# Performance work log

Measured on AMD Instinct MI355X. Metric: run time of the kernel, lower is better.

The kernel has to match this reference:

```python
import jax, jax.numpy as jnp
import numpy as np

N_NODES = 10000
N_EDGES = 160000
HID = 256
NBOND = 6
NATOM = 62
NLAYERS = 6


def _lin_init(key, fan_in, fan_out):
    # torch nn.Linear default: U(-1/sqrt(fan_in), 1/sqrt(fan_in))
    kw, kb = jax.random.split(key)
    bound = 1.0 / np.sqrt(fan_in)
    w = jax.random.uniform(kw, (fan_in, fan_out), jnp.float32, -bound, bound)
    b = jax.random.uniform(kb, (fan_out,), jnp.float32, -bound, bound)
    return w, b


def setup_inputs() -> dict:
    key = jax.random.key(0)
    ks = jax.random.split(key, 32)
    atom_features = jax.random.normal(ks[0], (N_NODES, NATOM), jnp.float32)
    edge_index = jax.random.randint(ks[1], (2, N_EDGES), 0, N_NODES, jnp.int64 if jax.config.jax_enable_x64 else jnp.int32)
    edge_features = jax.random.normal(ks[2], (N_EDGES, NBOND), jnp.float32)

    embed_w, embed_b = _lin_init(ks[3], NATOM, HID)

    msg_in = 2 * HID + NBOND  # 518
    mw1, mb1, mw2, mb2 = [], [], [], []
    uw1, ub1, uw2, ub2 = [], [], [], []
    for i in range(NLAYERS):
        k = jax.random.split(ks[4 + i], 4)
        w, b = _lin_init(k[0], msg_in, HID); mw1.append(w); mb1.append(b)
        w, b = _lin_init(k[1], HID, HID); mw2.append(w); mb2.append(b)
        w, b = _lin_init(k[2], 2 * HID, HID); uw1.append(w); ub1.append(b)
        w, b = _lin_init(k[3], HID, HID); uw2.append(w); ub2.append(b)

    r_w1, r_b1 = _lin_init(ks[20], HID, HID)
    r_w2, r_b2 = _lin_init(ks[21], HID, HID // 2)
    r_w3, r_b3 = _lin_init(ks[22], HID // 2, 1)

    return {
        "atom_features": atom_features,
        "edge_index": edge_index,
        "edge_features": edge_features,
        "embed_w": embed_w, "embed_b": embed_b,
        "msg_w1": jnp.stack(mw1), "msg_b1": jnp.stack(mb1),
        "msg_w2": jnp.stack(mw2), "msg_b2": jnp.stack(mb2),
        "upd_w1": jnp.stack(uw1), "upd_b1": jnp.stack(ub1),
        "upd_w2": jnp.stack(uw2), "upd_b2": jnp.stack(ub2),
        "r_w1": r_w1, "r_b1": r_b1,
        "r_w2": r_w2, "r_b2": r_b2,
        "r_w3": r_w3, "r_b3": r_b3,
    }


def _mlp2(x, w1, b1, w2, b2):
    return jnp.maximum(x @ w1 + b1, 0.0) @ w2 + b2


def reference(atom_features, edge_index, edge_features,
              embed_w, embed_b,
              msg_w1, msg_b1, msg_w2, msg_b2,
              upd_w1, upd_b1, upd_w2, upd_b2,
              r_w1, r_b1, r_w2, r_b2, r_w3, r_b3):
    src, dst = edge_index[0], edge_index[1]
    n = atom_features.shape[0]
    x = atom_features @ embed_w + embed_b  # [N, H]
    for l in range(msg_w1.shape[0]):
        # per-edge gather + concat -> message MLP
        msg_in = jnp.concatenate([x[src], x[dst], edge_features], axis=-1)  # [E, 2H+B]
        msgs = _mlp2(msg_in, msg_w1[l], msg_b1[l], msg_w2[l], msg_b2[l])  # [E, H]
        # scatter-add into dst nodes
        agg = jax.ops.segment_sum(msgs, dst, num_segments=n)  # [N, H]
        x = _mlp2(jnp.concatenate([x, agg], axis=-1), upd_w1[l], upd_b1[l], upd_w2[l], upd_b2[l])
    # readout (dropout is identity in eval mode)
    h = jnp.maximum(x @ r_w1 + r_b1, 0.0)
    h = jnp.maximum(h @ r_w2 + r_b2, 0.0)
    out = h @ r_w3 + r_b3  # [N, 1]
    return out.mean(axis=0)  # [1]
```

## Files before the change

kernel.cpp:

```cpp
#include <hip/hip_runtime.h>
#include <hip/hip_bf16.h>
#include <hip/hip_fp16.h>


#define HID 256

typedef _Float16 h8 __attribute__((ext_vector_type(8)));
typedef float f32x4 __attribute__((ext_vector_type(4)));

__device__ __forceinline__ void unpack_h8(const int4& r, float* f) {
    const __half2* h = reinterpret_cast<const __half2*>(&r);
#pragma unroll
    for (int k = 0; k < 4; ++k) {
        float2 t = __half22float2(h[k]);
        f[2 * k] = t.x;
        f[2 * k + 1] = t.y;
    }
}

__device__ __forceinline__ void unpack_h4(const int2& r, float* f) {
    const __half2* h = reinterpret_cast<const __half2*>(&r);
    float2 t0 = __half22float2(h[0]);
    float2 t1 = __half22float2(h[1]);
    f[0] = t0.x; f[1] = t0.y; f[2] = t1.x; f[3] = t1.y;
}

__device__ __forceinline__ void gld16(const void* g, void* l) {
    __builtin_amdgcn_global_load_lds(
        (const __attribute__((address_space(1))) void*)g,
        (__attribute__((address_space(3))) void*)l, 16, 0, 0);
}

__device__ __forceinline__ int swz(int row) { return (row + (row >> 2)) & 3; }


__global__ void hist_act_kernel(const int* __restrict__ dst, int* __restrict__ deg,
                                int E, const float* __restrict__ atom,
                                __half* __restrict__ atomH, int NA) {
    int i = blockIdx.x * blockDim.x + threadIdx.x;
    if (i < E) atomicAdd(&deg[dst[i]], 1);
    if (i < NA) {
        int r = i >> 3, seg = i & 7;
        h8 v;
#pragma unroll
        for (int j = 0; j < 8; ++j) {
            int c = seg * 8 + j;
            v[j] = (_Float16)((c < 62) ? atom[(size_t)r * 62 + c] : 0.f);
        }
        *reinterpret_cast<h8*>(&atomH[(size_t)r * 64 + seg * 8]) = v;
    }
}

__global__ __launch_bounds__(256) void scan_kernel(
    const int* __restrict__ deg, int* __restrict__ offs, float* __restrict__ degf, int n) {
    __shared__ int ws[4];
    const int t = threadIdx.x;
    const int lane = t & 63;
    const int w = t >> 6;
    const int per = (n + 255) / 256;
    const int s = t * per;
    const int e = min(s + per, n);
    int sum = 0;
    for (int i = s; i < e; ++i) sum += deg[i];
    int v = sum;
#pragma unroll
    for (int off = 1; off < 64; off <<= 1) {
        int u = __shfl_up(v, off, 64);
        if (lane >= off) v += u;
    }
    if (lane == 63) ws[w] = v;
    __syncthreads();
    if (t == 0) {
        int c = 0;
#pragma unroll
        for (int i = 0; i < 4; ++i) { int x = ws[i]; ws[i] = c; c += x; }
    }
    __syncthreads();
    int run = ws[w] + v - sum;
    for (int i = s; i < e; ++i) {
        int d = deg[i];
        offs[i] = run;
        degf[i] = (float)d;
        run += d;
    }
    if (e == n) offs[n] = run;
}


struct CDesc {
    const float* src;
    __half* dst;
    int Kreal, Kpad, srcN, tile0, dstStride;
};
struct CTab {
    CDesc d[32];
    int nd;
};

__device__ void convert_body(const CTab& tab, int bid) {
    int idx = 0;
    for (int i = 1; i < tab.nd; ++i)
        if (tab.d[i].tile0 <= bid) idx = i;
    const CDesc d = tab.d[idx];
    const int q = bid - d.tile0;
    const int ntN = d.srcN >> 6;
    const int kb = (q / ntN) * 32;
    const int nb = (q % ntN) * 64;
    const int n = nb + (threadIdx.x & 63);
    const int k0 = kb + (threadIdx.x >> 6) * 8;
    h8 v;
#pragma unroll
    for (int j = 0; j < 8; ++j) {
        int k = k0 + j;
        v[j] = (_Float16)((k < d.Kreal) ? d.src[(size_t)k * d.srcN + n] : 0.f);
    }
    *reinterpret_cast<h8*>(&d.dst[(size_t)n * d.dstStride + k0]) = v;
}

__global__ __launch_bounds__(256) void scatter_conv_kernel(
    const int* __restrict__ src, const int* __restrict__ dst,
    const int* __restrict__ offs, int* __restrict__ cursor,
    int* __restrict__ csr_src, const float* __restrict__ ef,
    __half* __restrict__ ef8, int E, int sblocks, CTab tab) {
    if ((int)blockIdx.x < sblocks) {
        int i = blockIdx.x * blockDim.x + threadIdx.x;
        if (i < E) {
            int d = dst[i];
            int pos = atomicAdd(&cursor[d], 1);
            int idx = offs[d] + pos;
            csr_src[idx] = src[i];
            const float* s6 = ef + (size_t)i * 6;
            unsigned short h[8];
#pragma unroll
            for (int j = 0; j < 6; ++j) h[j] = __half_as_ushort(__float2half_rn(s6[j]));
            h[6] = 0; h[7] = 0;
            int4 pk;
            pk.x = (int)(h[0] | ((unsigned)h[1] << 16));
            pk.y = (int)(h[2] | ((unsigned)h[3] << 16));
            pk.z = (int)(h[4] | ((unsigned)h[5] << 16));
            pk.w = (int)(h[6] | ((unsigned)h[7] << 16));
            *reinterpret_cast<int4*>(ef8 + (size_t)idx * 8) = pk;
        }
    } else {
        convert_body(tab, blockIdx.x - sblocks);
    }
}


struct BDesc { float* out; const float* base; const float* v1; const float* B1;
               const float* v2; const float* B2; };
struct BTab { BDesc d[31]; };


#define ASTR 40

struct FDesc { const float* U2; const __half* Wfb; __half* dst; int stride; };
struct FTab { FDesc d[22]; };

__device__ void fold_tile(unsigned char* ldsraw, const FDesc& dd, int t4) {
    _Float16* Ah = (_Float16*)ldsraw;
    _Float16* Bh = (_Float16*)(ldsraw + 64 * ASTR * 2);
    const int rowBase = (t4 >> 2) * 64;
    const int colBase = (t4 & 3) * 64;

    const int tid = threadIdx.x;
    const int lane = tid & 63;
    const int wave = tid >> 6;
    const int waveM = (wave >> 1) * 32;
    const int waveN = (wave & 1) * 32;
    const int m0 = lane & 15;
    const int quad = lane >> 4;
    const int sr = tid >> 2;
    const int sseg = tid & 3;

    const f32x4 z = {0.f, 0.f, 0.f, 0.f};
    f32x4 acc[2][2] = {{z, z}, {z, z}};

    for (int kb = 0; kb < 256; kb += 32) {
        {
            size_t off = (size_t)(rowBase + sr) * 256 + kb + sseg * 8;
            *reinterpret_cast<int4*>(&Ah[sr * ASTR + sseg * 8]) =
                *reinterpret_cast<const int4*>(&dd.Wfb[off]);
        }
        {
            const float* Bp = dd.U2 + (size_t)(colBase + sr) * 256 + kb + sseg * 8;
            float4 u0 = *reinterpret_cast<const float4*>(Bp);
            float4 u1 = *reinterpret_cast<const float4*>(Bp + 4);
            h8 v;
            v[0] = (_Float16)u0.x; v[1] = (_Float16)u0.y;
            v[2] = (_Float16)u0.z; v[3] = (_Float16)u0.w;
            v[4] = (_Float16)u1.x; v[5] = (_Float16)u1.y;
            v[6] = (_Float16)u1.z; v[7] = (_Float16)u1.w;
            *reinterpret_cast<h8*>(&Bh[sr * ASTR + sseg * 8]) = v;
        }
        __syncthreads();

        const h8 a0 = *reinterpret_cast<const h8*>(&Ah[(waveM + m0) * ASTR + quad * 8]);
        const h8 a1 = *reinterpret_cast<const h8*>(&Ah[(waveM + 16 + m0) * ASTR + quad * 8]);
        const h8 b0 = *reinterpret_cast<const h8*>(&Bh[(waveN + m0) * ASTR + quad * 8]);
        const h8 b1 = *reinterpret_cast<const h8*>(&Bh[(waveN + 16 + m0) * ASTR + quad * 8]);

        acc[0][0] = __builtin_amdgcn_mfma_f32_16x16x32_f16(a0, b0, acc[0][0], 0, 0, 0);
        acc[0][1] = __builtin_amdgcn_mfma_f32_16x16x32_f16(a0, b1, acc[0][1], 0, 0, 0);
        acc[1][0] = __builtin_amdgcn_mfma_f32_16x16x32_f16(a1, b0, acc[1][0], 0, 0, 0);
        acc[1][1] = __builtin_amdgcn_mfma_f32_16x16x32_f16(a1, b1, acc[1][1], 0, 0, 0);

        __syncthreads();
    }

#pragma unroll
    for (int tm = 0; tm < 2; ++tm)
#pragma unroll
        for (int reg = 0; reg < 4; ++reg) {
            int n = rowBase + waveM + tm * 16 + quad * 4 + reg;
#pragma unroll
            for (int tn = 0; tn < 2; ++tn) {
                int k = colBase + waveN + tn * 16 + m0;
                dd.dst[(size_t)n * dd.stride + k] = __float2half_rn(acc[tm][tn][reg]);
            }
        }
}


template <int TN>
__device__ void gemm_tile(
    unsigned char* lds, int bx, int by,
    const __half* __restrict__ A, int lda, const __half* __restrict__ A2,
    const __half* __restrict__ W, int K,
    const float* __restrict__ bias, const float* __restrict__ bias2,
    const float* __restrict__ rowscale,
    __half* __restrict__ C, int M, int Nc, int do_relu) {
    constexpr int BUF = 4096 + TN * 2048;

    const int tid = threadIdx.x;
    const int lane = tid & 63;
    const int wave = tid >> 6;
    const int m0 = lane & 15;
    const int quad = lane >> 4;
    const int waveM = (wave >> 1) * 32;
    const int waveN = (wave & 1) * (TN * 16);
    const int rowBase = bx * 64;
    const int colBase = by * (TN * 32);

    const int sa_r = tid >> 2;
    const int sa_ks = (tid & 3) ^ swz(sa_r);
    const int sa_row = min(rowBase + sa_r, M - 1);
    const int sb_r1 = sa_r + 64;
    const int sb_ks1 = (tid & 3) ^ swz(sb_r1);

    int aoff[2], boff[TN];
#pragma unroll
    for (int tm = 0; tm < 2; ++tm) {
        int r = waveM + tm * 16 + m0;
        aoff[tm] = ((r << 2) + (quad ^ swz(r))) << 4;
    }
#pragma unroll
    for (int tn = 0; tn < TN; ++tn) {
        int r = waveN + tn * 16 + m0;
        boff[tn] = 4096 + (((r << 2) + (quad ^ swz(r))) << 4);
    }

    const f32x4 z = {0.f, 0.f, 0.f, 0.f};
    f32x4 acc[2][TN];
#pragma unroll
    for (int tm = 0; tm < 2; ++tm)
#pragma unroll
        for (int tn = 0; tn < TN; ++tn) acc[tm][tn] = z;

    const __half* ga = A + (size_t)sa_row * lda + sa_ks * 8;
    const __half* ga2 = A2 ? A2 + (size_t)sa_row * lda + sa_ks * 8 : nullptr;
    const __half* gb0 = W + (size_t)(colBase + sa_r) * K + sa_ks * 8;
    const __half* gb1 = W + (size_t)(colBase + sb_r1) * K + sb_ks1 * 8;

    auto issue = [&](int p, int kb) {
        unsigned char* base = lds + p * BUF;
        const __half* as = (A2 && kb >= 256) ? (ga2 + (kb - 256)) : (ga + kb);
        gld16(as, base + wave * 1024);
        gld16(gb0 + kb, base + 4096 + wave * 1024);
        if constexpr (TN == 4) gld16(gb1 + kb, base + 8192 + wave * 1024);
    };

    issue(0, 0);
    int p = 0;
    for (int kb = 0; kb < K; kb += 32) {
        const bool has_next = (kb + 32 < K);
        if (has_next) issue(p ^ 1, kb + 32);
        if (has_next) {
            if constexpr (TN == 4)
                asm volatile("s_waitcnt vmcnt(3)" ::: "memory");
            else
                asm volatile("s_waitcnt vmcnt(2)" ::: "memory");
        } else {
            asm volatile("s_waitcnt vmcnt(0)" ::: "memory");
        }
        asm volatile("s_barrier" ::: "memory");

        const unsigned char* base = lds + p * BUF;
        h8 ah[2], bh[TN];
#pragma unroll
        for (int tm = 0; tm < 2; ++tm)
            ah[tm] = *reinterpret_cast<const h8*>(base + aoff[tm]);
#pragma unroll
        for (int tn = 0; tn < TN; ++tn)
            bh[tn] = *reinterpret_cast<const h8*>(base + boff[tn]);
#pragma unroll
        for (int tm = 0; tm < 2; ++tm)
#pragma unroll
            for (int tn = 0; tn < TN; ++tn)
                acc[tm][tn] = __builtin_amdgcn_mfma_f32_16x16x32_f16(
                    ah[tm], bh[tn], acc[tm][tn], 0, 0, 0);
        asm volatile("s_waitcnt lgkmcnt(0)" ::: "memory");
        asm volatile("s_barrier" ::: "memory");
        p ^= 1;
    }

    float cb[TN], db[TN];
    int col[TN];
#pragma unroll
    for (int tn = 0; tn < TN; ++tn) {
        col[tn] = colBase + waveN + tn * 16 + m0;
        cb[tn] = bias ? bias[col[tn]] : 0.f;
        db[tn] = bias2 ? bias2[col[tn]] : 0.f;
    }
#pragma unroll
    for (int tm = 0; tm < 2; ++tm) {
#pragma unroll
        for (int reg = 0; reg < 4; ++reg) {
            int row = rowBase + waveM + tm * 16 + quad * 4 + reg;
            if (row >= M) continue;
            float rs = rowscale ? rowscale[row] : 0.0f;
#pragma unroll
            for (int tn = 0; tn < TN; ++tn) {
                float v = acc[tm][tn][reg] + cb[tn] + rs * db[tn];
                if (do_relu) v = fmaxf(v, 0.f);
                C[(size_t)row * Nc + col[tn]] = __float2half_rn(v);
            }
        }
    }
}

template <int TN>
__global__ __launch_bounds__(256) void mfma_gemm(
    const __half* __restrict__ A, int lda, const __half* __restrict__ A2,
    const __half* __restrict__ W, int K,
    const float* __restrict__ bias, const float* __restrict__ bias2,
    const float* __restrict__ rowscale,
    __half* __restrict__ C, int M, int Nc, int do_relu) {
    __shared__ __align__(16) unsigned char lds[2 * (4096 + TN * 2048)];
    gemm_tile<TN>(lds, blockIdx.x, blockIdx.y, A, lda, A2, W, K,
                  bias, bias2, rowscale, C, M, Nc, do_relu);
}


__global__ __launch_bounds__(256) void fold_bias_embed_kernel(
    FTab ft, BTab bt, int fblocks, int bblocks,
    const __half* __restrict__ atomH, const __half* __restrict__ w_emb,
    const float* __restrict__ emb_b, __half* __restrict__ outX,
    int M, int mblk) {
    __shared__ __align__(16) unsigned char lds[16384];
    int b = blockIdx.x;
    if (b < fblocks) {
        fold_tile(lds, ft.d[b >> 4], b & 15);
        return;
    }
    b -= fblocks;
    if (b < bblocks) {
        const BDesc d = bt.d[b];
        const int j = threadIdx.x;
        float acc = d.base ? d.base[j] : 0.f;
        if (d.v1)
            for (int k = 0; k < 256; ++k) acc = fmaf(d.v1[k], d.B1[(size_t)k * 256 + j], acc);
        if (d.v2)
            for (int k = 0; k < 256; ++k) acc = fmaf(d.v2[k], d.B2[(size_t)k * 256 + j], acc);
        d.out[j] = acc;
        return;
    }
    b -= bblocks;
    gemm_tile<2>(lds, b % mblk, b / mblk, atomH, 64, nullptr, w_emb, 64,
                 emb_b, nullptr, nullptr, outX, M, HID, 0);
}


__global__ __launch_bounds__(256) void aggregate_kernel(
    const __half* __restrict__ PQ, const __half* __restrict__ ef8,
    const int* __restrict__ offs, const int* __restrict__ csr_src,
    const float* __restrict__ W1c, __half* __restrict__ Hagg, int n) {
    const int wave = threadIdx.x >> 6;
    const int lane = threadIdx.x & 63;
    const int node = blockIdx.x * 4 + wave;
    if (node >= n) return;
    const int ch = lane * 4;

    float wc[6][4];
#pragma unroll
    for (int k = 0; k < 6; ++k) {
        float4 w0 = *reinterpret_cast<const float4*>(W1c + k * HID + ch);
        wc[k][0] = w0.x; wc[k][1] = w0.y; wc[k][2] = w0.z; wc[k][3] = w0.w;
    }
    float qb[4];
    unpack_h4(*reinterpret_cast<const int2*>(PQ + (size_t)node * 512 + 256 + ch), qb);

    float acc[4] = {0.f, 0.f, 0.f, 0.f};

    auto fma_edge = [&](const int2& praw, const int4& eraw) {
        float p[4], e[8];
        unpack_h4(praw, p);
        unpack_h8(eraw, e);
#pragma unroll
        for (int i = 0; i < 4; ++i) {
            float h = p[i] + qb[i];
            h = fmaf(e[0], wc[0][i], h);
            h = fmaf(e[1], wc[1][i], h);
            h = fmaf(e[2], wc[2][i], h);
            h = fmaf(e[3], wc[3][i], h);
            h = fmaf(e[4], wc[4][i], h);
            h = fmaf(e[5], wc[5][i], h);
            acc[i] += fmaxf(h, 0.f);
        }
    };

    const int beg = offs[node];
    const int end = offs[node + 1];
    int j = beg;

    while (j + 6 <= end) {
        int s0 = csr_src[j];
        int s1 = csr_src[j + 1];
        int s2 = csr_src[j + 2];
        int s3 = csr_src[j + 3];
        int s4 = csr_src[j + 4];
        int s5 = csr_src[j + 5];
        int4 e0 = *reinterpret_cast<const int4*>(ef8 + (size_t)j * 8);
        int4 e1 = *reinterpret_cast<const int4*>(ef8 + (size_t)(j + 1) * 8);
        int4 e2 = *reinterpret_cast<const int4*>(ef8 + (size_t)(j + 2) * 8);
        int4 e3 = *reinterpret_cast<const int4*>(ef8 + (size_t)(j + 3) * 8);
        int4 e4 = *reinterpret_cast<const int4*>(ef8 + (size_t)(j + 4) * 8);
        int4 e5 = *reinterpret_cast<const int4*>(ef8 + (size_t)(j + 5) * 8);
        int2 p0 = *reinterpret_cast<const int2*>(PQ + (size_t)s0 * 512 + ch);
        int2 p1 = *reinterpret_cast<const int2*>(PQ + (size_t)s1 * 512 + ch);
        int2 p2 = *reinterpret_cast<const int2*>(PQ + (size_t)s2 * 512 + ch);
        int2 p3 = *reinterpret_cast<const int2*>(PQ + (size_t)s3 * 512 + ch);
        int2 p4 = *reinterpret_cast<const int2*>(PQ + (size_t)s4 * 512 + ch);
        int2 p5 = *reinterpret_cast<const int2*>(PQ + (size_t)s5 * 512 + ch);
        fma_edge(p0, e0);
        fma_edge(p1, e1);
        fma_edge(p2, e2);
        fma_edge(p3, e3);
        fma_edge(p4, e4);
        fma_edge(p5, e5);
        j += 6;
    }
    while (j + 2 <= end) {
        int s0 = csr_src[j];
        int s1 = csr_src[j + 1];
        int4 e0 = *reinterpret_cast<const int4*>(ef8 + (size_t)j * 8);
        int4 e1 = *reinterpret_cast<const int4*>(ef8 + (size_t)(j + 1) * 8);
        int2 p0 = *reinterpret_cast<const int2*>(PQ + (size_t)s0 * 512 + ch);
        int2 p1 = *reinterpret_cast<const int2*>(PQ + (size_t)s1 * 512 + ch);
        fma_edge(p0, e0);
        fma_edge(p1, e1);
        j += 2;
    }
    if (j < end) {
        int s = csr_src[j];
        int4 e = *reinterpret_cast<const int4*>(ef8 + (size_t)j * 8);
        int2 pw = *reinterpret_cast<const int2*>(PQ + (size_t)s * 512 + ch);
        fma_edge(pw, e);
    }

    unsigned short hs[4];
#pragma unroll
    for (int i = 0; i < 4; ++i) hs[i] = __half_as_ushort(__float2half_rn(acc[i]));
    int2 pk;
    pk.x = (int)(hs[0] | ((unsigned)hs[1] << 16));
    pk.y = (int)(hs[2] | ((unsigned)hs[3] << 16));
    *reinterpret_cast<int2*>(Hagg + (size_t)node * HID + ch) = pk;
}


__global__ __launch_bounds__(256) void readout_kernel(
    const __half* __restrict__ U5, const __half* __restrict__ wF,
    const float* __restrict__ cbF, const __half* __restrict__ wR2,
    const float* __restrict__ bR2, const float* __restrict__ w3,
    const float* __restrict__ b3, float* __restrict__ accum,
    int* __restrict__ done, float* __restrict__ outp, int M, int nblocks) {
    __shared__ __align__(16) unsigned char lds[24576 + 64 * 272 * 2];
    _Float16* h1 = (_Float16*)(lds + 24576);

    const int tid = threadIdx.x;
    const int lane = tid & 63;
    const int wave = tid >> 6;
    const int m0 = lane & 15;
    const int quad = lane >> 4;
    const int waveM = (wave >> 1) * 32;
    const int waveN = (wave & 1) * 64;
    const int rowBase = blockIdx.x * 64;

    const int sa_r = tid >> 2;
    const int sa_ks = (tid & 3) ^ swz(sa_r);
    const int sa_row = min(rowBase + sa_r, M - 1);
    const int sb_r1 = sa_r + 64;
    const int sb_ks1 = (tid & 3) ^ swz(sb_r1);

    int aoff[2], boff[4];
#pragma unroll
    for (int tm = 0; tm < 2; ++tm) {
        int r = waveM + tm * 16 + m0;
        aoff[tm] = ((r << 2) + (quad ^ swz(r))) << 4;
    }
#pragma unroll
    for (int tn = 0; tn < 4; ++tn) {
        int r = waveN + tn * 16 + m0;
        boff[tn] = (((r << 2) + (quad ^ swz(r))) << 4);
    }

    constexpr int BUF = 4096 + 4 * 2048;
    const f32x4 z = {0.f, 0.f, 0.f, 0.f};

    for (int half = 0; half < 2; ++half) {
        const __half* W = wF + (size_t)(half * 128) * 256;
        f32x4 acc[2][4] = {{z, z, z, z}, {z, z, z, z}};
        const __half* ga = U5 + (size_t)sa_row * 256 + sa_ks * 8;
        const __half* gb0 = W + (size_t)sa_r * 256 + sa_ks * 8;
        const __half* gb1 = W + (size_t)sb_r1 * 256 + sb_ks1 * 8;

        auto issue = [&](int p, int kb) {
            unsigned char* base = lds + p * BUF;
            gld16(ga + kb, base + wave * 1024);
            gld16(gb0 + kb, base + 4096 + wave * 1024);
            gld16(gb1 + kb, base + 8192 + wave * 1024);
        };
        issue(0, 0);
        int p = 0;
        for (int kb = 0; kb < 256; kb += 32) {
            const bool has_next = (kb + 32 < 256);
            if (has_next) issue(p ^ 1, kb + 32);
            if (has_next) asm volatile("s_waitcnt vmcnt(3)" ::: "memory");
            else asm volatile("s_waitcnt vmcnt(0)" ::: "memory");
            asm volatile("s_barrier" ::: "memory");
            const unsigned char* base = lds + p * BUF;
            h8 ah[2], bh[4];
#pragma unroll
            for (int tm = 0; tm < 2; ++tm)
                ah[tm] = *reinterpret_cast<const h8*>(base + aoff[tm]);
#pragma unroll
            for (int tn = 0; tn < 4; ++tn)
                bh[tn] = *reinterpret_cast<const h8*>(base + 4096 + boff[tn]);
#pragma unroll
            for (int tm = 0; tm < 2; ++tm)
#pragma unroll
                for (int tn = 0; tn < 4; ++tn)
                    acc[tm][tn] = __builtin_amdgcn_mfma_f32_16x16x32_f16(
                        ah[tm], bh[tn], acc[tm][tn], 0, 0, 0);
            asm volatile("s_waitcnt lgkmcnt(0)" ::: "memory");
            asm volatile("s_barrier" ::: "memory");
            p ^= 1;
        }
#pragma unroll
        for (int tm = 0; tm < 2; ++tm)
#pragma unroll
            for (int reg = 0; reg < 4; ++reg) {
                int r = waveM + tm * 16 + quad * 4 + reg;
#pragma unroll
                for (int tn = 0; tn < 4; ++tn) {
                    int c = half * 128 + waveN + tn * 16 + m0;
                    float v = acc[tm][tn][reg] + cbF[c];
                    h1[r * 272 + c] = (_Float16)fmaxf(v, 0.f);
                }
            }
        __syncthreads();
    }

    f32x4 acc2[2][4] = {{z, z, z, z}, {z, z, z, z}};
    auto issueB = [&](int p, int kb) {
        unsigned char* base = lds + p * 8192;
        gld16(wR2 + (size_t)sa_r * 256 + sa_ks * 8 + kb, base + wave * 1024);
        gld16(wR2 + (size_t)sb_r1 * 256 + sb_ks1 * 8 + kb, base + 4096 + wave * 1024);
    };
    issueB(0, 0);
    int p = 0;
    for (int kb = 0; kb < 256; kb += 32) {
        const bool has_next = (kb + 32 < 256);
        if (has_next) issueB(p ^ 1, kb + 32);
        if (has_next) asm volatile("s_waitcnt vmcnt(2)" ::: "memory");
        else asm volatile("s_waitcnt vmcnt(0)" ::: "memory");
        asm volatile("s_barrier" ::: "memory");
        const unsigned char* base = lds + p * 8192;
        h8 ah[2], bh[4];
#pragma unroll
        for (int tm = 0; tm < 2; ++tm)
            ah[tm] = *reinterpret_cast<const h8*>(
                &h1[(waveM + tm * 16 + m0) * 272 + kb + quad * 8]);
#pragma unroll
        for (int tn = 0; tn < 4; ++tn)
            bh[tn] = *reinterpret_cast<const h8*>(base + boff[tn]);
#pragma unroll
        for (int tm = 0; tm < 2; ++tm)
#pragma unroll
            for (int tn = 0; tn < 4; ++tn)
                acc2[tm][tn] = __builtin_amdgcn_mfma_f32_16x16x32_f16(
                    ah[tm], bh[tn], acc2[tm][tn], 0, 0, 0);
        asm volatile("s_waitcnt lgkmcnt(0)" ::: "memory");
        asm volatile("s_barrier" ::: "memory");
        p ^= 1;
    }

    float s = 0.f;
#pragma unroll
    for (int tm = 0; tm < 2; ++tm)
#pragma unroll
        for (int reg = 0; reg < 4; ++reg) {
            int row = rowBase + waveM + tm * 16 + quad * 4 + reg;
            if (row >= M) continue;
#pragma unroll
            for (int tn = 0; tn < 4; ++tn) {
                int c = waveN + tn * 16 + m0;
                float v = acc2[tm][tn][reg] + bR2[c];
                s += fmaxf(v, 0.f) * w3[c];
            }
        }
    __syncthreads();
    float* red = (float*)lds;
    red[tid] = s;
    __syncthreads();
    for (int off = 128; off > 0; off >>= 1) {
        if (tid < off) red[tid] += red[tid + off];
        __syncthreads();
    }
    if (tid == 0) {
        atomicAdd(accum, red[0]);
        __threadfence();
        int old = atomicAdd(done, 1);
        if (old == nblocks - 1) {
            float tot = atomicAdd(accum, 0.0f);
            outp[0] = tot / (float)M + b3[0];
        }
    }
}


extern "C" void kernel_launch(void* const* d_in, const int* in_sizes, int n_in,
                              void* d_out, int out_size, void* d_ws, size_t ws_size,
                              hipStream_t stream) {
    const float* atom   = (const float*)d_in[0];
    const int*   eidx   = (const int*)d_in[1];
    const float* ef     = (const float*)d_in[2];
    const float* emb_w  = (const float*)d_in[3];
    const float* emb_b  = (const float*)d_in[4];
    const float* msg_w1 = (const float*)d_in[5];
    const float* msg_b1 = (const float*)d_in[6];
    const float* msg_w2 = (const float*)d_in[7];
    const float* msg_b2 = (const float*)d_in[8];
    const float* upd_w1 = (const float*)d_in[9];
    const float* upd_b1 = (const float*)d_in[10];
    const float* upd_w2 = (const float*)d_in[11];
    const float* upd_b2 = (const float*)d_in[12];
    const float* r_w1   = (const float*)d_in[13];
    const float* r_b1   = (const float*)d_in[14];
    const float* r_w2   = (const float*)d_in[15];
    const float* r_b2   = (const float*)d_in[16];
    const float* r_w3   = (const float*)d_in[17];
    const float* r_b3   = (const float*)d_in[18];

    const int N = in_sizes[0] / 62;
    const int E = in_sizes[1] / 2;
    const int L = in_sizes[5] / (518 * 256);
    const int* src = eidx;
    const int* dst = eidx + E;

    char* wp = (char*)d_ws;
    auto alloc = [&](size_t bytes) -> void* {
        void* p = (void*)wp;
        wp += (bytes + 255) & ~(size_t)255;
        return p;
    };
    int*   deg     = (int*)alloc((size_t)N * 4);
    int*   cursor  = (int*)alloc((size_t)N * 4);
    float* accum   = (float*)alloc(256);
    int*   done    = (int*)((char*)accum + 16);
    size_t zero_bytes = (size_t)((char*)accum - (char*)d_ws) + 256;
    float* degf    = (float*)alloc((size_t)N * 4);
    int*   offs    = (int*)alloc((size_t)(N + 1) * 4);
    int*   csr_src = (int*)alloc((size_t)E * 4);
    __half* ef8    = (__half*)alloc((size_t)E * 8 * 2);

    const int SQ_P = 256 * 256;
    __half* w_emb = (__half*)alloc((size_t)256 * 64 * 2);
    __half* w_r2  = (__half*)alloc((size_t)128 * 256 * 2);
    __half* wF    = (__half*)alloc((size_t)SQ_P * 2);
    __half *wPQ[6], *wUPD[6];
    for (int l = 0; l < L; ++l) {
        wPQ[l]  = (__half*)alloc((size_t)512 * 256 * 2);
        wUPD[l] = (__half*)alloc((size_t)256 * 512 * 2);
    }
    __half* fb[22];
    for (int i = 0; i < 22; ++i) fb[i] = (__half*)alloc((size_t)SQ_P * 2);
    float* bvec = (float*)alloc((size_t)19 * 256 * 4);
    float* b512 = (float*)alloc((size_t)L * 512 * 4);

    __half* atomH = (__half*)alloc((size_t)N * 64 * 2);
    __half* bufX0 = (__half*)alloc((size_t)N * HID * 2);
    __half* bufX1 = (__half*)alloc((size_t)N * HID * 2);
    __half* PQ    = (__half*)alloc((size_t)N * 512 * 2);
    __half* HaggH = (__half*)alloc((size_t)N * HID * 2);

    hipMemsetAsync(d_ws, 0, zero_bytes, stream);

    const int hag = max(E, N * 8);
    hist_act_kernel<<<(hag + 255) / 256, 256, 0, stream>>>(dst, deg, E, atom, atomH, N * 8);
    scan_kernel<<<1, 256, 0, stream>>>(deg, offs, degf, N);

    CTab ct1;
    int nd = 0, tiles = 0;
    auto addDesc = [&](const float* s, __half* dh, int Kreal, int Kpad, int srcN,
                       int dstStride) {
        ct1.d[nd] = {s, dh, Kreal, Kpad, srcN, tiles, dstStride};
        tiles += (Kpad / 32) * (srcN / 64);
        ++nd;
    };
    addDesc(emb_w, w_emb, 62, 64, 256, 64);
    addDesc(msg_w1, wPQ[0], 256, 256, 256, 256);
    addDesc(msg_w1 + 256 * 256, wPQ[0] + SQ_P, 256, 256, 256, 256);
    addDesc(upd_w1, wUPD[0] + 256, 256, 256, 256, 512);
    addDesc(r_w2, w_r2, 256, 256, 128, 256);
    for (int l = 1; l < L; ++l) {
        addDesc(msg_w1 + (size_t)l * 518 * 256,             fb[l - 1], 256, 256, 256, 256);
        addDesc(msg_w1 + (size_t)l * 518 * 256 + 256 * 256, fb[4 + l], 256, 256, 256, 256);
        addDesc(upd_w1 + (size_t)l * 512 * 256,             fb[9 + l], 256, 256, 256, 256);
    }
    for (int l = 0; l < L; ++l)
        addDesc(upd_w1 + (size_t)l * 512 * 256 + 256 * 256, fb[15 + l], 256, 256, 256, 256);
    addDesc(r_w1, fb[21], 256, 256, 256, 256);
    ct1.nd = nd;

    const int sblocks = (E + 255) / 256;
    scatter_conv_kernel<<<sblocks + tiles, 256, 0, stream>>>(
        src, dst, offs, cursor, csr_src, ef, ef8, E, sblocks, ct1);

    FTab ft;
    for (int l = 1; l < L; ++l) {
        const float* U2p = upd_w2 + (size_t)(l - 1) * SQ_P;
        ft.d[l - 1] = {U2p, fb[l - 1], wPQ[l], 256};
        ft.d[4 + l] = {U2p, fb[4 + l], wPQ[l] + SQ_P, 256};
        ft.d[9 + l] = {U2p, fb[9 + l], wUPD[l] + 256, 512};
    }
    for (int l = 0; l < L; ++l)
        ft.d[15 + l] = {msg_w2 + (size_t)l * SQ_P, fb[15 + l], wUPD[l], 512};
    ft.d[21] = {upd_w2 + (size_t)5 * SQ_P, fb[21], wF, 256};

    BTab bt;
    int nb = 0;
    for (int l = 0; l < L; ++l) {
        const float* ub2p = (l > 0) ? upd_b2 + (size_t)(l - 1) * 256 : nullptr;
        bt.d[nb++] = {b512 + (size_t)l * 512 + 256, msg_b1 + (size_t)l * 256,
                      ub2p, msg_w1 + (size_t)l * 518 * 256,
                      ub2p, msg_w1 + (size_t)l * 518 * 256 + 256 * 256};
        bt.d[nb++] = {b512 + (size_t)l * 512, nullptr, nullptr, nullptr, nullptr, nullptr};
        bt.d[nb++] = {bvec + (size_t)(6 + l) * 256, upd_b1 + (size_t)l * 256,
                      ub2p, upd_w1 + (size_t)l * 512 * 256, nullptr, nullptr};
        bt.d[nb++] = {bvec + (size_t)(12 + l) * 256, nullptr,
                      msg_b2 + (size_t)l * 256, upd_w1 + (size_t)l * 512 * 256 + 256 * 256,
                      nullptr, nullptr};
    }
    bt.d[nb++] = {bvec + (size_t)18 * 256, r_b1, upd_b2 + (size_t)5 * 256, r_w1,
                  nullptr, nullptr};

    const int mblk = (N + 63) / 64;
    const int fblocks = 22 * 16;
    fold_bias_embed_kernel<<<fblocks + nb + mblk * 4, 256, 0, stream>>>(
        ft, bt, fblocks, nb, atomH, w_emb, emb_b, bufX0, N, mblk);

    dim3 blk(256);
    __half* U_prev = bufX0;
    __half* U_next = bufX1;
    for (int l = 0; l < L; ++l) {
        const float* w1c = msg_w1 + (size_t)l * 518 * 256 + 512 * 256;

        mfma_gemm<4><<<dim3(mblk, 4), blk, 0, stream>>>(
            U_prev, HID, nullptr, wPQ[l], HID,
            b512 + (size_t)l * 512, nullptr, nullptr,
            PQ, N, 512, 0);
        aggregate_kernel<<<(N + 3) / 4, blk, 0, stream>>>(
            PQ, ef8, offs, csr_src, w1c, HaggH, N);
        mfma_gemm<2><<<dim3(mblk, 4), blk, 0, stream>>>(
            HaggH, HID, U_prev, wUPD[l], 512,
            bvec + (size_t)(6 + l) * 256, bvec + (size_t)(12 + l) * 256, degf,
            U_next, N, HID, 1);
        __half* t = U_prev; U_prev = U_next; U_next = t;
    }

    readout_kernel<<<mblk, blk, 0, stream>>>(
        U_prev, wF, bvec + (size_t)18 * 256, w_r2, r_b2, r_w3, r_b3,
        accum, done, (float*)d_out, N, mblk);
}
```

Before: 446.6 us.

## Use 128x128 MFMA GEMM tiles for layer GEMMs and re-fuse setup kernels

Replaces the per-layer 64-row GEMMs with a new gemm128 kernel that computes 128x128 output tiles, each wave holding a 4x4 grid of 16x16 MFMA accumulators. This raises operand reuse per LDS load, at the cost of fewer blocks (about 79 row tiles) and more registers per thread. Setup work is also regrouped: the weight conversion moves into the histogram kernel, and the CSR scatter merges with the fold/bias/embed kernel. This removes one launch from the preprocessing chain.

Result: slower. 464.5 us (+4.0%).

```diff
diff --git a/kernel.cpp b/kernel.cpp
--- a/kernel.cpp
+++ b/kernel.cpp
@@ -34,20 +34,56 @@
 __device__ __forceinline__ int swz(int row) { return (row + (row >> 2)) & 3; }
 
 
-__global__ void hist_act_kernel(const int* __restrict__ dst, int* __restrict__ deg,
-                                int E, const float* __restrict__ atom,
-                                __half* __restrict__ atomH, int NA) {
-    int i = blockIdx.x * blockDim.x + threadIdx.x;
-    if (i < E) atomicAdd(&deg[dst[i]], 1);
-    if (i < NA) {
-        int r = i >> 3, seg = i & 7;
-        h8 v;
-#pragma unroll
-        for (int j = 0; j < 8; ++j) {
-            int c = seg * 8 + j;
-            v[j] = (_Float16)((c < 62) ? atom[(size_t)r * 62 + c] : 0.f);
-        }
-        *reinterpret_cast<h8*>(&atomH[(size_t)r * 64 + seg * 8]) = v;
+struct CDesc {
+    const float* src;
+    __half* dst;
+    int Kreal, Kpad, srcN, tile0, dstStride;
+};
+struct CTab {
+    CDesc d[32];
+    int nd;
+};
+
+__device__ void convert_body(const CTab& tab, int bid) {
+    int idx = 0;
+    for (int i = 1; i < tab.nd; ++i)
+        if (tab.d[i].tile0 <= bid) idx = i;
+    const CDesc d = tab.d[idx];
+    const int q = bid - d.tile0;
+    const int ntN = d.srcN >> 6;
+    const int kb = (q / ntN) * 32;
+    const int nb = (q % ntN) * 64;
+    const int n = nb + (threadIdx.x & 63);
+    const int k0 = kb + (threadIdx.x >> 6) * 8;
+    h8 v;
+#pragma unroll
+    for (int j = 0; j < 8; ++j) {
+        int k = k0 + j;
+        v[j] = (_Float16)((k < d.Kreal) ? d.src[(size_t)k * d.srcN + n] : 0.f);
+    }
+    *reinterpret_cast<h8*>(&d.dst[(size_t)n * d.dstStride + k0]) = v;
+}
+
+
+__global__ void hist_conv_kernel(const int* __restrict__ dst, int* __restrict__ deg,
+                                 int E, const float* __restrict__ atom,
+                                 __half* __restrict__ atomH, int NA,
+                                 int histB, CTab tab) {
+    if ((int)blockIdx.x < histB) {
+        int i = blockIdx.x * blockDim.x + threadIdx.x;
+        if (i < E) atomicAdd(&deg[dst[i]], 1);
+        if (i < NA) {
+            int r = i >> 3, seg = i & 7;
+            h8 v;
+#pragma unroll
+            for (int j = 0; j < 8; ++j) {
+                int c = seg * 8 + j;
+                v[j] = (_Float16)((c < 62) ? atom[(size_t)r * 62 + c] : 0.f);
+            }
+            *reinterpret_cast<h8*>(&atomH[(size_t)r * 64 + seg * 8]) = v;
+        }
+    } else {
+        convert_body(tab, blockIdx.x - histB);
     }
 }
 
@@ -87,66 +123,6 @@
 }
 
 
-struct CDesc {
-    const float* src;
-    __half* dst;
-    int Kreal, Kpad, srcN, tile0, dstStride;
-};
-struct CTab {
-    CDesc d[32];
-    int nd;
-};
-
-__device__ void convert_body(const CTab& tab, int bid) {
-    int idx = 0;
-    for (int i = 1; i < tab.nd; ++i)
-        if (tab.d[i].tile0 <= bid) idx = i;
-    const CDesc d = tab.d[idx];
-    const int q = bid - d.tile0;
-    const int ntN = d.srcN >> 6;
-    const int kb = (q / ntN) * 32;
-    const int nb = (q % ntN) * 64;
-    const int n = nb + (threadIdx.x & 63);
-    const int k0 = kb + (threadIdx.x >> 6) * 8;
-    h8 v;
-#pragma unroll
-    for (int j = 0; j < 8; ++j) {
-        int k = k0 + j;
-        v[j] = (_Float16)((k < d.Kreal) ? d.src[(size_t)k * d.srcN + n] : 0.f);
-    }
-    *reinterpret_cast<h8*>(&d.dst[(size_t)n * d.dstStride + k0]) = v;
-}
-
-__global__ __launch_bounds__(256) void scatter_conv_kernel(
-    const int* __restrict__ src, const int* __restrict__ dst,
-    const int* __restrict__ offs, int* __restrict__ cursor,
-    int* __restrict__ csr_src, const float* __restrict__ ef,
-    __half* __restrict__ ef8, int E, int sblocks, CTab tab) {
-    if ((int)blockIdx.x < sblocks) {
-        int i = blockIdx.x * blockDim.x + threadIdx.x;
-        if (i < E) {
-            int d = dst[i];
-            int pos = atomicAdd(&cursor[d], 1);
-            int idx = offs[d] + pos;
-            csr_src[idx] = src[i];
-            const float* s6 = ef + (size_t)i * 6;
-            unsigned short h[8];
-#pragma unroll
-            for (int j = 0; j < 6; ++j) h[j] = __half_as_ushort(__float2half_rn(s6[j]));
-            h[6] = 0; h[7] = 0;
-            int4 pk;
-            pk.x = (int)(h[0] | ((unsigned)h[1] << 16));
-            pk.y = (int)(h[2] | ((unsigned)h[3] << 16));
-            pk.z = (int)(h[4] | ((unsigned)h[5] << 16));
-            pk.w = (int)(h[6] | ((unsigned)h[7] << 16));
-            *reinterpret_cast<int4*>(ef8 + (size_t)idx * 8) = pk;
-        }
-    } else {
-        convert_body(tab, blockIdx.x - sblocks);
-    }
-}
-
-
 struct BDesc { float* out; const float* base; const float* v1; const float* B1;
                const float* v2; const float* B2; };
 struct BTab { BDesc d[31]; };
@@ -225,10 +201,9 @@
 template <int TN>
 __device__ void gemm_tile(
     unsigned char* lds, int bx, int by,
-    const __half* __restrict__ A, int lda, const __half* __restrict__ A2,
+    const __half* __restrict__ A, int lda,
     const __half* __restrict__ W, int K,
-    const float* __restrict__ bias, const float* __restrict__ bias2,
-    const float* __restrict__ rowscale,
+    const float* __restrict__ bias,
     __half* __restrict__ C, int M, int Nc, int do_relu) {
     constexpr int BUF = 4096 + TN * 2048;
 
@@ -268,14 +243,12 @@
         for (int tn = 0; tn < TN; ++tn) acc[tm][tn] = z;
 
     const __half* ga = A + (size_t)sa_row * lda + sa_ks * 8;
-    const __half* ga2 = A2 ? A2 + (size_t)sa_row * lda + sa_ks * 8 : nullptr;
     const __half* gb0 = W + (size_t)(colBase + sa_r) * K + sa_ks * 8;
     const __half* gb1 = W + (size_t)(colBase + sb_r1) * K + sb_ks1 * 8;
 
     auto issue = [&](int p, int kb) {
         unsigned char* base = lds + p * BUF;
-        const __half* as = (A2 && kb >= 256) ? (ga2 + (kb - 256)) : (ga + kb);
-        gld16(as, base + wave * 1024);
+        gld16(ga + kb, base + wave * 1024);
         gld16(gb0 + kb, base + 4096 + wave * 1024);
         if constexpr (TN == 4) gld16(gb1 + kb, base + 8192 + wave * 1024);
     };
@@ -314,13 +287,12 @@
         p ^= 1;
     }
 
-    float cb[TN], db[TN];
+    float cb[TN];
     int col[TN];
 #pragma unroll
     for (int tn = 0; tn < TN; ++tn) {
         col[tn] = colBase + waveN + tn * 16 + m0;
         cb[tn] = bias ? bias[col[tn]] : 0.f;
-        db[tn] = bias2 ? bias2[col[tn]] : 0.f;
     }
 #pragma unroll
     for (int tm = 0; tm < 2; ++tm) {
@@ -328,10 +300,9 @@
         for (int reg = 0; reg < 4; ++reg) {
             int row = rowBase + waveM + tm * 16 + quad * 4 + reg;
             if (row >= M) continue;
-            float rs = rowscale ? rowscale[row] : 0.0f;
 #pragma unroll
             for (int tn = 0; tn < TN; ++tn) {
-                float v = acc[tm][tn][reg] + cb[tn] + rs * db[tn];
+                float v = acc[tm][tn][reg] + cb[tn];
                 if (do_relu) v = fmaxf(v, 0.f);
                 C[(size_t)row * Nc + col[tn]] = __float2half_rn(v);
             }
@@ -339,26 +310,40 @@
     }
 }
 
-template <int TN>
-__global__ __launch_bounds__(256) void mfma_gemm(
-    const __half* __restrict__ A, int lda, const __half* __restrict__ A2,
-    const __half* __restrict__ W, int K,
-    const float* __restrict__ bias, const float* __restrict__ bias2,
-    const float* __restrict__ rowscale,
-    __half* __restrict__ C, int M, int Nc, int do_relu) {
-    __shared__ __align__(16) unsigned char lds[2 * (4096 + TN * 2048)];
-    gemm_tile<TN>(lds, blockIdx.x, blockIdx.y, A, lda, A2, W, K,
-                  bias, bias2, rowscale, C, M, Nc, do_relu);
-}
-
-
-__global__ __launch_bounds__(256) void fold_bias_embed_kernel(
+
+__global__ __launch_bounds__(256) void scatter_fold_bias_embed_kernel(
+    const int* __restrict__ src, const int* __restrict__ dst,
+    const int* __restrict__ offs, int* __restrict__ cursor,
+    int* __restrict__ csr_src, const float* __restrict__ ef,
+    __half* __restrict__ ef8, int E, int sblocks,
     FTab ft, BTab bt, int fblocks, int bblocks,
     const __half* __restrict__ atomH, const __half* __restrict__ w_emb,
     const float* __restrict__ emb_b, __half* __restrict__ outX,
-    int M, int mblk) {
+    int M, int mblk64) {
     __shared__ __align__(16) unsigned char lds[16384];
     int b = blockIdx.x;
+    if (b < sblocks) {
+        int i = b * 256 + (int)threadIdx.x;
+        if (i < E) {
+            int d = dst[i];
+            int pos = atomicAdd(&cursor[d], 1);
+            int idx = offs[d] + pos;
+            csr_src[idx] = src[i];
+            const float* s6 = ef + (size_t)i * 6;
+            unsigned short h[8];
+#pragma unroll
+            for (int j = 0; j < 6; ++j) h[j] = __half_as_ushort(__float2half_rn(s6[j]));
+            h[6] = 0; h[7] = 0;
+            int4 pk;
+            pk.x = (int)(h[0] | ((unsigned)h[1] << 16));
+            pk.y = (int)(h[2] | ((unsigned)h[3] << 16));
+            pk.z = (int)(h[4] | ((unsigned)h[5] << 16));
+            pk.w = (int)(h[6] | ((unsigned)h[7] << 16));
+            *reinterpret_cast<int4*>(ef8 + (size_t)idx * 8) = pk;
+        }
+        return;
+    }
+    b -= sblocks;
     if (b < fblocks) {
         fold_tile(lds, ft.d[b >> 4], b & 15);
         return;
@@ -376,8 +361,123 @@
         return;
     }
     b -= bblocks;
-    gemm_tile<2>(lds, b % mblk, b / mblk, atomH, 64, nullptr, w_emb, 64,
-                 emb_b, nullptr, nullptr, outX, M, HID, 0);
+    gemm_tile<2>(lds, b % mblk64, b / mblk64, atomH, 64, w_emb, 64,
+                 emb_b, outX, M, HID, 0);
+}
+
+
+__global__ __launch_bounds__(256) void gemm128(
+    const __half* __restrict__ A, int lda, const __half* __restrict__ A2,
+    const __half* __restrict__ W, int K,
+    const float* __restrict__ bias, const float* __restrict__ bias2,
+    const float* __restrict__ rowscale,
+    __half* __restrict__ C, int M, int Nc, int do_relu) {
+    __shared__ __align__(16) unsigned char lds[2 * 16384];
+
+    const int tid = threadIdx.x;
+    const int lane = tid & 63;
+    const int wave = tid >> 6;
+    const int m0 = lane & 15;
+    const int quad = lane >> 4;
+    const int waveM = (wave >> 1) * 64;
+    const int waveN = (wave & 1) * 64;
+    const int rowBase = (int)blockIdx.x * 128;
+    const int colBase = (int)blockIdx.y * 128;
+
+    const __half* ga[2];
+    const __half* ga2[2];
+    const __half* gb[2];
+    int adst[2], bdst[2];
+#pragma unroll
+    for (int j = 0; j < 2; ++j) {
+        int seg = j * 256 + wave * 64 + lane;
+        int r = seg >> 2;
+        int ks = (seg & 3) ^ swz(r);
+        int arow = min(rowBase + r, M - 1);
+        ga[j] = A + (size_t)arow * lda + ks * 8;
+        ga2[j] = A2 ? A2 + (size_t)arow * lda + ks * 8 : nullptr;
+        gb[j] = W + (size_t)(colBase + r) * K + ks * 8;
+        adst[j] = (j * 4 + wave) * 1024;
+        bdst[j] = 8192 + (j * 4 + wave) * 1024;
+    }
+
+    int aoff[4], boff[4];
+#pragma unroll
+    for (int i = 0; i < 4; ++i) {
+        int r = waveM + i * 16 + m0;
+        aoff[i] = ((r << 2) + (quad ^ swz(r))) << 4;
+        int rb = waveN + i * 16 + m0;
+        boff[i] = 8192 + (((rb << 2) + (quad ^ swz(rb))) << 4);
+    }
+
+    const f32x4 z = {0.f, 0.f, 0.f, 0.f};
+    f32x4 acc[4][4];
+#pragma unroll
+    for (int i = 0; i < 4; ++i)
+#pragma unroll
+        for (int j = 0; j < 4; ++j) acc[i][j] = z;
+
+    auto issue = [&](int p, int kb) {
+        unsigned char* base = lds + p * 16384;
+        const bool hi = (A2 != nullptr) && (kb >= 256);
+        const int ko = hi ? (kb - 256) : kb;
+#pragma unroll
+        for (int j = 0; j < 2; ++j)
+            gld16((hi ? ga2[j] : ga[j]) + ko, base + adst[j]);
+#pragma unroll
+        for (int j = 0; j < 2; ++j)
+            gld16(gb[j] + kb, base + bdst[j]);
+    };
+
+    issue(0, 0);
+    int p = 0;
+    for (int kb = 0; kb < K; kb += 32) {
+        const bool has_next = (kb + 32 < K);
+        if (has_next) issue(p ^ 1, kb + 32);
+        if (has_next) asm volatile("s_waitcnt vmcnt(4)" ::: "memory");
+        else          asm volatile("s_waitcnt vmcnt(0)" ::: "memory");
+        asm volatile("s_barrier" ::: "memory");
+
+        const unsigned char* base = lds + p * 16384;
+        h8 ah[4], bh[4];
+#pragma unroll
+        for (int i = 0; i < 4; ++i) ah[i] = *reinterpret_cast<const h8*>(base + aoff[i]);
+#pragma unroll
+        for (int j = 0; j < 4; ++j) bh[j] = *reinterpret_cast<const h8*>(base + boff[j]);
+#pragma unroll
+        for (int i = 0; i < 4; ++i)
+#pragma unroll
+            for (int j = 0; j < 4; ++j)
+                acc[i][j] = __builtin_amdgcn_mfma_f32_16x16x32_f16(
+                    ah[i], bh[j], acc[i][j], 0, 0, 0);
+        asm volatile("s_waitcnt lgkmcnt(0)" ::: "memory");
+        asm volatile("s_barrier" ::: "memory");
+        p ^= 1;
+    }
+
+    float cb[4], db[4];
+    int col[4];
+#pragma unroll
+    for (int j = 0; j < 4; ++j) {
+        col[j] = colBase + waveN + j * 16 + m0;
+        cb[j] = bias ? bias[col[j]] : 0.f;
+        db[j] = bias2 ? bias2[col[j]] : 0.f;
+    }
+#pragma unroll
+    for (int i = 0; i < 4; ++i) {
+#pragma unroll
+        for (int reg = 0; reg < 4; ++reg) {
+            int row = rowBase + waveM + i * 16 + quad * 4 + reg;
+            if (row >= M) continue;
+            float rs = rowscale ? rowscale[row] : 0.0f;
+#pragma unroll
+            for (int j = 0; j < 4; ++j) {
+                float v = acc[i][j][reg] + cb[j] + rs * db[j];
+                if (do_relu) v = fmaxf(v, 0.f);
+                C[(size_t)row * Nc + col[j]] = __float2half_rn(v);
+            }
+        }
+    }
 }
 
 
@@ -706,10 +806,6 @@
 
     hipMemsetAsync(d_ws, 0, zero_bytes, stream);
 
-    const int hag = max(E, N * 8);
-    hist_act_kernel<<<(hag + 255) / 256, 256, 0, stream>>>(dst, deg, E, atom, atomH, N * 8);
-    scan_kernel<<<1, 256, 0, stream>>>(deg, offs, degf, N);
-
     CTab ct1;
     int nd = 0, tiles = 0;
     auto addDesc = [&](const float* s, __half* dh, int Kreal, int Kpad, int srcN,
@@ -733,9 +829,12 @@
     addDesc(r_w1, fb[21], 256, 256, 256, 256);
     ct1.nd = nd;
 
-    const int sblocks = (E + 255) / 256;
-    scatter_conv_kernel<<<sblocks + tiles, 256, 0, stream>>>(
-        src, dst, offs, cursor, csr_src, ef, ef8, E, sblocks, ct1);
+    const int hag = max(E, N * 8);
+    const int histB = (hag + 255) / 256;
+    hist_conv_kernel<<<histB + tiles, 256, 0, stream>>>(
+        dst, deg, E, atom, atomH, N * 8, histB, ct1);
+
+    scan_kernel<<<1, 256, 0, stream>>>(deg, offs, degf, N);
 
     FTab ft;
     for (int l = 1; l < L; ++l) {
@@ -765,31 +864,34 @@
     bt.d[nb++] = {bvec + (size_t)18 * 256, r_b1, upd_b2 + (size_t)5 * 256, r_w1,
                   nullptr, nullptr};
 
-    const int mblk = (N + 63) / 64;
+    const int sblocks = (E + 255) / 256;
     const int fblocks = 22 * 16;
-    fold_bias_embed_kernel<<<fblocks + nb + mblk * 4, 256, 0, stream>>>(
-        ft, bt, fblocks, nb, atomH, w_emb, emb_b, bufX0, N, mblk);
-
-    dim3 blk(256);
+    const int mblk64 = (N + 63) / 64;
+    scatter_fold_bias_embed_kernel<<<sblocks + fblocks + nb + mblk64 * 4, 256, 0,
+                                     stream>>>(
+        src, dst, offs, cursor, csr_src, ef, ef8, E, sblocks,
+        ft, bt, fblocks, nb, atomH, w_emb, emb_b, bufX0, N, mblk64);
+
+    const int mblkR = (N + 127) / 128;
     __half* U_prev = bufX0;
     __half* U_next = bufX1;
     for (int l = 0; l < L; ++l) {
         const float* w1c = msg_w1 + (size_t)l * 518 * 256 + 512 * 256;
 
-        mfma_gemm<4><<<dim3(mblk, 4), blk, 0, stream>>>(
+        gemm128<<<dim3(mblkR, 4), 256, 0, stream>>>(
             U_prev, HID, nullptr, wPQ[l], HID,
             b512 + (size_t)l * 512, nullptr, nullptr,
             PQ, N, 512, 0);
-        aggregate_kernel<<<(N + 3) / 4, blk, 0, stream>>>(
+        aggregate_kernel<<<(N + 3) / 4, 256, 0, stream>>>(
             PQ, ef8, offs, csr_src, w1c, HaggH, N);
-        mfma_gemm<2><<<dim3(mblk, 4), blk, 0, stream>>>(
+        gemm128<<<dim3(mblkR, 2), 256, 0, stream>>>(
             HaggH, HID, U_prev, wUPD[l], 512,
             bvec + (size_t)(6 + l) * 256, bvec + (size_t)(12 + l) * 256, degf,
-            U_next, N, HID, 1);
+            U_next, N, 256, 1);
         __half* t = U_prev; U_prev = U_next; U_next = t;
     }
 
-    readout_kernel<<<mblk, blk, 0, stream>>>(
+    readout_kernel<<<mblk64, 256, 0, stream>>>(
         U_prev, wF, bvec + (size_t)18 * 256, w_r2, r_b2, r_w3, r_b3,
-        accum, done, (float*)d_out, N, mblk);
-}
+        accum, done, (float*)d_out, N, mblk64);
+}
```
